# Optimization experiments

Hardware: AMD Instinct MI355X
Metric: run time of the kernel (lower is better)

## Reference

```python
import jax, jax.numpy as jnp
import numpy as np

P = 2        # patch size (all 3 dims)
NB = 8       # num_bands
N = 16       # d_state
DTR = 8      # dt_rank = d_model // 16
DCONV = 4    # d_conv
SMAX = 2.0   # smax_dt = smax_B = smax_C


def _ln(x, g, b):
    mu = x.mean(-1, keepdims=True)
    v = ((x - mu) ** 2).mean(-1, keepdims=True)
    return (x - mu) / jnp.sqrt(v + 1e-5) * g + b


def _silu(x):
    return x * jax.nn.sigmoid(x)


def _ssm_layer(x, band, m, rho, Win, bin_, convw, convb, Wx, Wdt, bdt, Alog, Dp,
               Wout, bout, edt, eB, eC, wr, wm):
    # x: [B, L, d_model] -> bidirectional conditioned selective scan (BiFCSSM)
    Bsz, L, _ = x.shape
    ED = convw.shape[0]
    xz = x @ Win + bin_
    xp, z = xz[..., :ED], xz[..., ED:]
    # depthwise causal conv1d over L
    xpad = jnp.pad(xp, ((0, 0), (DCONV - 1, 0), (0, 0)))
    xc = sum(xpad[:, k:k + L, :] * convw[:, k] for k in range(DCONV)) + convb
    xc = _silu(xc)
    dbl = xc @ Wx                                    # [B,L,DTR+2N]
    dt = jax.nn.softplus(dbl[..., :DTR] @ Wdt + bdt)  # [B,L,ED]
    # band/radius/mask conditioned modulation of delta, B, C
    s_dt = SMAX * jax.nn.sigmoid(edt[band][None] + wr[0] * rho[None] + wm[0] * m)
    s_B = SMAX * jax.nn.sigmoid(eB[band][None] + wr[1] * rho[None] + wm[1] * m)
    s_C = SMAX * jax.nn.sigmoid(eC[band][None] + wr[2] * rho[None] + wm[2] * m)
    dt = dt * s_dt[..., None]
    Bm = dbl[..., DTR:DTR + N] * s_B[..., None]       # [B,L,N]
    Cm = dbl[..., DTR + N:] * s_C[..., None]          # [B,L,N]
    A = -jnp.exp(Alog)                                # [ED,N]
    dA = jnp.exp(dt[..., None] * A)                   # [B,L,ED,N]
    dBu = (dA - 1.0) / A * Bm[:, :, None, :] * xc[..., None]   # exact ZOH
    dA_s = jnp.moveaxis(dA, 1, 0)
    dBu_s = jnp.moveaxis(dBu, 1, 0)
    C_s = jnp.moveaxis(Cm, 1, 0)
    h0 = jnp.zeros((Bsz, ED, N), x.dtype)

    def step(h, inp):
        a, bu, c = inp
        h = a * h + bu
        return h, jnp.einsum('ben,bn->be', h, c)

    _, yf = jax.lax.scan(step, h0, (dA_s, dBu_s, C_s))
    _, yb = jax.lax.scan(step, h0, (dA_s, dBu_s, C_s), reverse=True)
    y = jnp.moveaxis(yf + yb, 0, 1) + Dp * xc
    y = y * _silu(z)
    return y @ Wout + bout


def _fwd(kspace_ri, mask, pe_w, pe_b, pu_w, pu_b, ln_g, ln_b, fn_g, fn_b,
         cond_band, cond_rad_w, cond_mask_w, l0_Win, l0_bin, l0_convw, l0_convb,
         l0_Wx, l0_Wdt, l0_bdt, l0_Alog, l0_D, l0_Wout, l0_bout, l0_edt, l0_eB,
         l0_eC, l0_wr, l0_wm):
    Bsz, C, nx, ny, nz = kspace_ri.shape
    gx, gy, gz = nx // P, ny // P, nz // P
    L = gx * gy * gz
    # patch embed (Conv3d, kernel==stride) as blocked einsum
    xr = kspace_ri.reshape(Bsz, C, gx, P, gy, P, gz, P)
    x = jnp.einsum('bcxiyjzk,dcijk->bdxyz', xr, pe_w) + pe_b[None, :, None, None, None]
    DM = x.shape[1]
    x = x.reshape(Bsz, DM, L).transpose(0, 2, 1)               # [B,L,D]
    m = mask.reshape(Bsz, 1, gx, P, gy, P, gz, P).mean(axis=(3, 5, 7)).reshape(Bsz, L)
    m = jnp.clip(m, 0.0, 1.0)
    # raster scan ordering: identity permutation, rho_bar, band ids
    rho = jnp.arange(L, dtype=x.dtype) / float(L - 1)
    band = jnp.clip(jnp.floor(rho * NB).astype(jnp.int32), 0, NB - 1)
    # condition tokens
    cond = cond_band[band][None] + rho[None, :, None] * cond_rad_w + m[:, :, None] * cond_mask_w
    h = _ln(x + cond, ln_g, ln_b)
    h = h + _ssm_layer(_ln(h, fn_g, fn_b), band, m, rho, l0_Win, l0_bin, l0_convw,
                       l0_convb, l0_Wx, l0_Wdt, l0_bdt, l0_Alog, l0_D, l0_Wout,
                       l0_bout, l0_edt, l0_eB, l0_eC, l0_wr, l0_wm)
    # patch unembed (ConvTranspose3d, kernel==stride) as blocked einsum
    hg = h.transpose(0, 2, 1).reshape(Bsz, DM, gx, gy, gz)
    out = jnp.einsum('bdxyz,dcijk->bcxiyjzk', hg, pu_w).reshape(Bsz, C, nx, ny, nz)
    out = out + pu_b[None, :, None, None, None]
    return kspace_ri + out


def setup_inputs() -> dict:
    key = jax.random.key(0)
    ks = jax.random.split(key, 24)
    ED, DM, CIN = 256, 128, 16

    def nrm(k, shape, s):
        return jax.random.normal(k, shape, jnp.float32) * s

    return {
        'kspace_ri': jax.random.normal(ks[0], (1, CIN, 64, 64, 16), jnp.float32),
        'mask': jax.random.uniform(ks[1], (1, 1, 64, 64, 16), jnp.float32),
        'pe_w': nrm(ks[2], (DM, CIN, P, P, P), 0.09),
        'pe_b': nrm(ks[3], (DM,), 0.02),
        'pu_w': nrm(ks[4], (DM, CIN, P, P, P), 0.05),
        'pu_b': jnp.zeros((CIN,), jnp.float32),
        'ln_g': jnp.ones((DM,), jnp.float32),
        'ln_b': jnp.zeros((DM,), jnp.float32),
        'fn_g': jnp.ones((DM,), jnp.float32),
        'fn_b': jnp.zeros((DM,), jnp.float32),
        'cond_band': nrm(ks[5], (NB, DM), 0.02),
        'cond_rad_w': nrm(ks[6], (DM,), 0.02),
        'cond_mask_w': nrm(ks[7], (DM,), 0.02),
        'l0_Win': nrm(ks[8], (DM, 2 * ED), 0.05),
        'l0_bin': jnp.zeros((2 * ED,), jnp.float32),
        'l0_convw': nrm(ks[9], (ED, DCONV), 0.2),
        'l0_convb': jnp.zeros((ED,), jnp.float32),
        'l0_Wx': nrm(ks[10], (ED, DTR + 2 * N), 0.05),
        'l0_Wdt': nrm(ks[11], (DTR, ED), 0.1),
        'l0_bdt': jnp.full((ED,), -3.0, jnp.float32),
        'l0_Alog': jnp.log(jnp.tile(jnp.arange(1, N + 1, dtype=jnp.float32), (ED, 1))),
        'l0_D': jnp.ones((ED,), jnp.float32),
        'l0_Wout': nrm(ks[12], (ED, DM), 0.05),
        'l0_bout': jnp.zeros((DM,), jnp.float32),
        'l0_edt': nrm(ks[13], (NB,), 0.1),
        'l0_eB': nrm(ks[14], (NB,), 0.1),
        'l0_eC': nrm(ks[15], (NB,), 0.1),
        'l0_wr': nrm(ks[16], (3,), 0.1),
        'l0_wm': nrm(ks[17], (3,), 0.1),
    }


def reference(kspace_ri, mask, pe_w, pe_b, pu_w, pu_b, ln_g, ln_b, fn_g, fn_b,
              cond_band, cond_rad_w, cond_mask_w, l0_Win, l0_bin, l0_convw,
              l0_convb, l0_Wx, l0_Wdt, l0_bdt, l0_Alog, l0_D, l0_Wout, l0_bout,
              l0_edt, l0_eB, l0_eC, l0_wr, l0_wm):
    return _fwd(kspace_ri, mask, pe_w, pe_b, pu_w, pu_b, ln_g, ln_b, fn_g, fn_b,
                cond_band, cond_rad_w, cond_mask_w, l0_Win, l0_bin, l0_convw,
                l0_convb, l0_Wx, l0_Wdt, l0_bdt, l0_Alog, l0_D, l0_Wout, l0_bout,
                l0_edt, l0_eB, l0_eC, l0_wr, l0_wm)
```

## Files before the change

kernel.cpp:

```cpp
#include <hip/hip_runtime.h>
#include <hip/hip_bf16.h>

#define L_TOK 8192
#define NCh 256
#define CLh 32
#define LOG2E 1.44269504088896f

typedef short bf16x8 __attribute__((ext_vector_type(8)));
typedef float f32x4 __attribute__((ext_vector_type(4)));

static __device__ __forceinline__ float nexp2(float x) {
#if __has_builtin(__builtin_amdgcn_exp2f)
    return __builtin_amdgcn_exp2f(x);
#else
    return exp2f(x);
#endif
}
static __device__ __forceinline__ float sigm(float x) {
    return 1.f / (1.f + nexp2(-x * LOG2E));
}
static __device__ __forceinline__ ushort f2bf(float x) {
    union { float f; uint u; } v; v.f = x;
    uint r = v.u + 0x7fffu + ((v.u >> 16) & 1u);
    return (ushort)(r >> 16);
}
static __device__ __forceinline__ float bf2f(ushort h) {
    union { float f; uint u; } v; v.u = ((uint)h) << 16;
    return v.f;
}
static __device__ __forceinline__ void f2hl(float x, ushort* hi, ushort* lo) {
    ushort h = f2bf(x);
    *hi = h;
    *lo = f2bf(x - bf2f(h));
}

#define W_PE   0
#define W_WIN  16384
#define W_WOUT 81920
#define W_PU   114688
#define W_PROJ 131072
#define W_TOT  212992

__global__ __launch_bounds__(256) void prep_k(const float* __restrict__ pe_w, const float* __restrict__ Win,
                                              const float* __restrict__ Wx, const float* __restrict__ Wdt,
                                              const float* __restrict__ Wout, const float* __restrict__ pu_w,
                                              const float* __restrict__ mask,
                                              ushort* __restrict__ wH, ushort* __restrict__ wL,
                                              float* __restrict__ mbuf) {
    int b = blockIdx.x;
    if (b >= 832) {
        int l = (b - 832) * 256 + threadIdx.x;
        int xg = l >> 8, yg = (l >> 3) & 31, zg = l & 7;
        float s = 0.f;
        for (int i2 = 0; i2 < 2; ++i2)
            for (int j2 = 0; j2 < 2; ++j2)
                for (int k2 = 0; k2 < 2; ++k2)
                    s += mask[(2 * xg + i2) * 1024 + (2 * yg + j2) * 16 + 2 * zg + k2];
        s *= 0.125f;
        mbuf[l] = fminf(fmaxf(s, 0.f), 1.f);
        return;
    }
    int i = b * 256 + threadIdx.x;
    float v;
    if (i < 16384) {
        v = pe_w[i];
    } else if (i < 81920) {
        int j = i - 16384; int n = j >> 7, k = j & 127;
        v = Win[k * 512 + n];
    } else if (i < 114688) {
        int j = i - 81920; int n = j >> 8, k = j & 255;
        v = Wout[k * 128 + n];
    } else if (i < 131072) {
        int j = i - 114688; int n = j >> 7, k = j & 127;
        v = pu_w[k * 128 + n];
    } else {
        int j = i - 131072; int n = j >> 8, k = j & 255;
        if (n < 256) {
            float s = 0.f;
#pragma unroll
            for (int r = 0; r < 8; ++r) s += Wx[k * 40 + r] * Wdt[r * 256 + n];
            v = s;
        } else if (n < 288) {
            v = Wx[k * 40 + 8 + (n - 256)];
        } else {
            v = 0.f;
        }
    }
    ushort h, lo; f2hl(v, &h, &lo);
    wH[i] = h; wL[i] = lo;
}

__global__ __launch_bounds__(256) void embed_ln_k(const float* __restrict__ ks,
                                                  const ushort* __restrict__ wH, const ushort* __restrict__ wL,
                                                  const float* __restrict__ pe_b, const float* __restrict__ cond_band,
                                                  const float* __restrict__ cond_rad, const float* __restrict__ cond_mask,
                                                  const float* __restrict__ mbuf,
                                                  const float* __restrict__ ln_g, const float* __restrict__ ln_b,
                                                  const float* __restrict__ fn_g, const float* __restrict__ fn_b,
                                                  float* __restrict__ h_,
                                                  ushort* __restrict__ hnH, ushort* __restrict__ hnL) {
    __shared__ __align__(16) char smem[50176];
    ushort (*AsH)[72] = (ushort(*)[72])(smem);
    ushort (*AsL)[72] = (ushort(*)[72])(smem + 2304);
    ushort (*BsH)[72] = (ushort(*)[72])(smem + 4608);
    ushort (*BsL)[72] = (ushort(*)[72])(smem + 23040);
    float*  ksb       = (float*)(smem + 41472);
    float  (*Cs)[132] = (float(*)[132])(smem);

    const int tid = threadIdx.x;
    const int lane = tid & 63, wn = tid >> 6;
    const int ln = lane & 15, q = lane >> 4;
    const int mb = blockIdx.x * 16;
    const int xg = mb >> 8, yg0 = (mb >> 3) & 31;

    for (int v = tid; v < 512; v += 256) {
        int seg = v >> 2, zq = v & 3;
        int cc = seg >> 3, i2 = (seg >> 2) & 1, yy = seg & 3;
        float4 t4 = *(const float4*)&ks[cc * 65536 + (2 * xg + i2) * 1024 + (2 * yg0 + yy) * 16 + zq * 4];
        int la = seg * 17 + zq * 4;
        ksb[la] = t4.x; ksb[la + 1] = t4.y; ksb[la + 2] = t4.z; ksb[la + 3] = t4.w;
    }

    f32x4 acc[2];
    acc[0] = (f32x4){0.f, 0.f, 0.f, 0.f};
    acc[1] = (f32x4){0.f, 0.f, 0.f, 0.f};

    for (int kc = 0; kc < 128; kc += 64) {
        __syncthreads();
        for (int u = tid; u < 1024; u += 256) {
            int r = u >> 6, kk = u & 63;
            int k = kc + kk;
            int cc = k >> 3, ijk = k & 7;
            int i2 = (ijk >> 2) & 1, j2 = (ijk >> 1) & 1, k2 = ijk & 1;
            int seg = (cc * 2 + i2) * 4 + (r >> 3) * 2 + j2;
            float v = ksb[seg * 17 + (r & 7) * 2 + k2];
            ushort hh, ll; f2hl(v, &hh, &ll);
            AsH[r][kk] = hh; AsL[r][kk] = ll;
        }
        for (int u = tid; u < 1024; u += 256) {
            int n = u >> 3, g = u & 7;
            *(uint4*)&BsH[n][g * 8] = *(const uint4*)&wH[W_PE + n * 128 + kc + g * 8];
            *(uint4*)&BsL[n][g * 8] = *(const uint4*)&wL[W_PE + n * 128 + kc + g * 8];
        }
        __syncthreads();
#pragma unroll
        for (int ks_ = 0; ks_ < 64; ks_ += 32) {
            const int kk = ks_ + q * 8;
            bf16x8 ah = *(const bf16x8*)&AsH[ln][kk];
            bf16x8 al = *(const bf16x8*)&AsL[ln][kk];
#pragma unroll
            for (int cb = 0; cb < 2; ++cb) {
                bf16x8 bh = *(const bf16x8*)&BsH[wn * 32 + cb * 16 + ln][kk];
                bf16x8 bl = *(const bf16x8*)&BsL[wn * 32 + cb * 16 + ln][kk];
                acc[cb] = __builtin_amdgcn_mfma_f32_16x16x32_bf16(ah, bh, acc[cb], 0, 0, 0);
                acc[cb] = __builtin_amdgcn_mfma_f32_16x16x32_bf16(ah, bl, acc[cb], 0, 0, 0);
                acc[cb] = __builtin_amdgcn_mfma_f32_16x16x32_bf16(al, bh, acc[cb], 0, 0, 0);
            }
        }
    }
    __syncthreads();
#pragma unroll
    for (int cb = 0; cb < 2; ++cb) {
#pragma unroll
        for (int r = 0; r < 4; ++r) {
            int row = q * 4 + r;
            int col = wn * 32 + cb * 16 + ln;
            int l = mb + row;
            float rho = (float)l * (1.0f / 8191.0f);
            int band = min(7, (int)(rho * 8.0f));
            Cs[row][col] = acc[cb][r] + pe_b[col] + cond_band[band * 128 + col]
                           + rho * cond_rad[col] + mbuf[l] * cond_mask[col];
        }
    }
    __syncthreads();
    {
        int row = tid >> 4, j = tid & 15;
        int l = mb + row;
        float v8[8];
        float s = 0.f, s2 = 0.f;
#pragma unroll
        for (int i = 0; i < 8; ++i) {
            float v = Cs[row][j * 8 + i];
            v8[i] = v; s += v; s2 += v * v;
        }
#pragma unroll
        for (int o = 1; o < 16; o <<= 1) { s += __shfl_xor(s, o, 16); s2 += __shfl_xor(s2, o, 16); }
        float mu = s * (1.f / 128.f);
        float var = s2 * (1.f / 128.f) - mu * mu;
        float rstd = rsqrtf(fmaxf(var, 0.f) + 1e-5f);
        float hv[8];
        s = 0.f; s2 = 0.f;
#pragma unroll
        for (int i = 0; i < 8; ++i) {
            int col = j * 8 + i;
            float h = (v8[i] - mu) * rstd * ln_g[col] + ln_b[col];
            hv[i] = h; s += h; s2 += h * h;
        }
#pragma unroll
        for (int i = 0; i < 8; i += 4)
            *(float4*)&h_[(size_t)l * 128 + j * 8 + i] = make_float4(hv[i], hv[i + 1], hv[i + 2], hv[i + 3]);
#pragma unroll
        for (int o = 1; o < 16; o <<= 1) { s += __shfl_xor(s, o, 16); s2 += __shfl_xor(s2, o, 16); }
        mu = s * (1.f / 128.f);
        var = s2 * (1.f / 128.f) - mu * mu;
        rstd = rsqrtf(fmaxf(var, 0.f) + 1e-5f);
        union { ushort u[8]; uint4 v4; } oh, ol;
#pragma unroll
        for (int i = 0; i < 8; ++i) {
            int col = j * 8 + i;
            float o2 = (hv[i] - mu) * rstd * fn_g[col] + fn_b[col];
            ushort hh, ll; f2hl(o2, &hh, &ll);
            oh.u[i] = hh; ol.u[i] = ll;
        }
        *(uint4*)&hnH[(size_t)l * 128 + j * 8] = oh.v4;
        *(uint4*)&hnL[(size_t)l * 128 + j * 8] = ol.v4;
    }
}

__global__ __launch_bounds__(256) void win_k(const ushort* __restrict__ Ah, const ushort* __restrict__ Al,
                                             const ushort* __restrict__ wH, const ushort* __restrict__ wL,
                                             const float* __restrict__ bin_,
                                             float* __restrict__ xp, float* __restrict__ sz) {
    __shared__ ushort AsH[64][72], AsL[64][72];
    __shared__ ushort BsH[64][72], BsL[64][72];
    const int tid = threadIdx.x;
    const int lane = tid & 63, wave = tid >> 6;
    const int wm = wave & 1, wn = wave >> 1;
    const int ln = lane & 15, q = lane >> 4;
    const int mb = blockIdx.x * 64, nb = blockIdx.y * 64;

    f32x4 acc[2][2];
#pragma unroll
    for (int rb = 0; rb < 2; ++rb)
#pragma unroll
        for (int cb = 0; cb < 2; ++cb) acc[rb][cb] = (f32x4){0.f, 0.f, 0.f, 0.f};

    for (int kc = 0; kc < 128; kc += 64) {
        __syncthreads();
        for (int u = tid; u < 512; u += 256) {
            int r = u >> 3, g = u & 7;
            size_t go = (size_t)(mb + r) * 128 + kc + g * 8;
            *(uint4*)&AsH[r][g * 8] = *(const uint4*)&Ah[go];
            *(uint4*)&AsL[r][g * 8] = *(const uint4*)&Al[go];
        }
        for (int u = tid; u < 512; u += 256) {
            int n = u >> 3, g = u & 7;
            size_t go = (size_t)(W_WIN) + (size_t)(nb + n) * 128 + kc + g * 8;
            *(uint4*)&BsH[n][g * 8] = *(const uint4*)&wH[go];
            *(uint4*)&BsL[n][g * 8] = *(const uint4*)&wL[go];
        }
        __syncthreads();
#pragma unroll
        for (int ks_ = 0; ks_ < 64; ks_ += 32) {
            const int kk = ks_ + q * 8;
            bf16x8 ah[2], al[2], bh[2], bl[2];
#pragma unroll
            for (int rb = 0; rb < 2; ++rb) {
                ah[rb] = *(const bf16x8*)&AsH[wm * 32 + rb * 16 + ln][kk];
                al[rb] = *(const bf16x8*)&AsL[wm * 32 + rb * 16 + ln][kk];
            }
#pragma unroll
            for (int cb = 0; cb < 2; ++cb) {
                bh[cb] = *(const bf16x8*)&BsH[wn * 32 + cb * 16 + ln][kk];
                bl[cb] = *(const bf16x8*)&BsL[wn * 32 + cb * 16 + ln][kk];
            }
#pragma unroll
            for (int rb = 0; rb < 2; ++rb)
#pragma unroll
                for (int cb = 0; cb < 2; ++cb) {
                    acc[rb][cb] = __builtin_amdgcn_mfma_f32_16x16x32_bf16(ah[rb], bh[cb], acc[rb][cb], 0, 0, 0);
                    acc[rb][cb] = __builtin_amdgcn_mfma_f32_16x16x32_bf16(ah[rb], bl[cb], acc[rb][cb], 0, 0, 0);
                    acc[rb][cb] = __builtin_amdgcn_mfma_f32_16x16x32_bf16(al[rb], bh[cb], acc[rb][cb], 0, 0, 0);
                }
        }
    }
#pragma unroll
    for (int rb = 0; rb < 2; ++rb)
#pragma unroll
        for (int cb = 0; cb < 2; ++cb)
#pragma unroll
            for (int r = 0; r < 4; ++r) {
                int l = mb + wm * 32 + rb * 16 + q * 4 + r;
                int col = nb + wn * 32 + cb * 16 + ln;
                float v = acc[rb][cb][r] + bin_[col];
                if (col < 256) {
                    xp[(size_t)l * 256 + col] = v;
                } else {
                    sz[(size_t)l * 256 + (col - 256)] = v * sigm(v);
                }
            }
}

__global__ __launch_bounds__(512) void proj_k(const float* __restrict__ xp,
                                              const float* __restrict__ convw, const float* __restrict__ convb,
                                              const ushort* __restrict__ wH, const ushort* __restrict__ wL,
                                              const float* __restrict__ bdt, const float* __restrict__ mbuf,
                                              const float* __restrict__ edt, const float* __restrict__ eB,
                                              const float* __restrict__ eC, const float* __restrict__ wr,
                                              const float* __restrict__ wm,
                                              float* __restrict__ xc, float* __restrict__ dt,
                                              float* __restrict__ Bm, float* __restrict__ Cm) {
    __shared__ __align__(16) char smem[52224];
    ushort (*AsH)[264] = (ushort(*)[264])(smem);
    ushort (*AsL)[264] = (ushort(*)[264])(smem + 16896);
    ushort (*BsH)[72]  = (ushort(*)[72])(smem + 33792);
    ushort (*BsL)[72]  = (ushort(*)[72])(smem + 43008);
    const int tid = threadIdx.x;
    const int mb = blockIdx.x * 32;

    {
        const int cg = tid & 63;
        const int rg = tid >> 6;
        const int c0 = cg * 4;
        float4 cb4 = *(const float4*)&convb[c0];
        float4 cw0 = *(const float4*)&convw[(c0 + 0) * 4];
        float4 cw1 = *(const float4*)&convw[(c0 + 1) * 4];
        float4 cw2 = *(const float4*)&convw[(c0 + 2) * 4];
        float4 cw3 = *(const float4*)&convw[(c0 + 3) * 4];
        const int lbase = mb + rg * 4;
        float4 zero = make_float4(0.f, 0.f, 0.f, 0.f);
        float4 x0 = (lbase - 3 >= 0) ? *(const float4*)&xp[(size_t)(lbase - 3) * 256 + c0] : zero;
        float4 x1 = (lbase - 2 >= 0) ? *(const float4*)&xp[(size_t)(lbase - 2) * 256 + c0] : zero;
        float4 x2 = (lbase - 1 >= 0) ? *(const float4*)&xp[(size_t)(lbase - 1) * 256 + c0] : zero;
#pragma unroll
        for (int rr = 0; rr < 4; ++rr) {
            int l = lbase + rr;
            float4 x3 = *(const float4*)&xp[(size_t)l * 256 + c0];
            float o0 = cb4.x + x0.x * cw0.x + x1.x * cw0.y + x2.x * cw0.z + x3.x * cw0.w;
            float o1 = cb4.y + x0.y * cw1.x + x1.y * cw1.y + x2.y * cw1.z + x3.y * cw1.w;
            float o2 = cb4.z + x0.z * cw2.x + x1.z * cw2.y + x2.z * cw2.z + x3.z * cw2.w;
            float o3 = cb4.w + x0.w * cw3.x + x1.w * cw3.y + x2.w * cw3.z + x3.w * cw3.w;
            o0 *= sigm(o0); o1 *= sigm(o1); o2 *= sigm(o2); o3 *= sigm(o3);
            *(float4*)&xc[(size_t)l * 256 + c0] = make_float4(o0, o1, o2, o3);
            union { ushort u[4]; uint2 v2; } hh, ll;
            f2hl(o0, &hh.u[0], &ll.u[0]); f2hl(o1, &hh.u[1], &ll.u[1]);
            f2hl(o2, &hh.u[2], &ll.u[2]); f2hl(o3, &hh.u[3], &ll.u[3]);
            int row = l - mb;
            *(uint2*)&AsH[row][c0] = hh.v2;
            *(uint2*)&AsL[row][c0] = ll.v2;
            x0 = x1; x1 = x2; x2 = x3;
        }
    }
    __syncthreads();

    const int lane = tid & 63, wave = tid >> 6;
    const int wm2 = wave & 1, wn4 = wave >> 1;
    const int ln = lane & 15, q = lane >> 4;
    for (int it = 0; it < 5; ++it) {
        int nb = it * 64;
        f32x4 acc = (f32x4){0.f, 0.f, 0.f, 0.f};
        for (int kc = 0; kc < 256; kc += 64) {
            __syncthreads();
            {
                int u = tid;
                int n = u >> 3, g = u & 7;
                size_t go = (size_t)(W_PROJ) + (size_t)(nb + n) * 256 + kc + g * 8;
                *(uint4*)&BsH[n][g * 8] = *(const uint4*)&wH[go];
                *(uint4*)&BsL[n][g * 8] = *(const uint4*)&wL[go];
            }
            __syncthreads();
#pragma unroll
            for (int ks_ = 0; ks_ < 64; ks_ += 32) {
                const int kka = kc + ks_ + q * 8;
                const int kkb = ks_ + q * 8;
                bf16x8 ah = *(const bf16x8*)&AsH[wm2 * 16 + ln][kka];
                bf16x8 al = *(const bf16x8*)&AsL[wm2 * 16 + ln][kka];
                bf16x8 bh = *(const bf16x8*)&BsH[wn4 * 16 + ln][kkb];
                bf16x8 bl = *(const bf16x8*)&BsL[wn4 * 16 + ln][kkb];
                acc = __builtin_amdgcn_mfma_f32_16x16x32_bf16(ah, bh, acc, 0, 0, 0);
                acc = __builtin_amdgcn_mfma_f32_16x16x32_bf16(ah, bl, acc, 0, 0, 0);
                acc = __builtin_amdgcn_mfma_f32_16x16x32_bf16(al, bh, acc, 0, 0, 0);
            }
        }
#pragma unroll
        for (int r = 0; r < 4; ++r) {
            int l = mb + wm2 * 16 + q * 4 + r;
            int col = nb + wn4 * 16 + ln;
            float v = acc[r];
            float rho = (float)l * (1.0f / 8191.0f);
            int band = min(7, (int)(rho * 8.0f));
            float mv = mbuf[l];
            if (col < 256) {
                float sc0 = 2.0f * sigm(edt[band] + wr[0] * rho + wm[0] * mv);
                float v2 = v + bdt[col];
                float sp = (v2 > 20.f) ? v2 : log1pf(expf(v2));
                dt[(size_t)l * 256 + col] = sp * sc0;
            } else if (col < 272) {
                float sc1 = 2.0f * sigm(eB[band] + wr[1] * rho + wm[1] * mv);
                Bm[(size_t)l * 16 + (col - 256)] = v * sc1;
            } else if (col < 288) {
                float sc2 = 2.0f * sigm(eC[band] + wr[2] * rho + wm[2] * mv);
                Cm[(size_t)l * 16 + (col - 272)] = v * sc2;
            }
        }
    }
}

__global__ __launch_bounds__(256) void scan0_k(const float* __restrict__ dt, const float* __restrict__ xc,
                                               const float* __restrict__ Bm, const float* __restrict__ Alog,
                                               float* __restrict__ Hb, float* __restrict__ sdtb) {
    const int c = blockIdx.x, dir = blockIdx.y, e = threadIdx.x;
    __shared__ float bms[CLh][16];
    for (int idx = e; idx < CLh * 16; idx += 256)
        bms[idx >> 4][idx & 15] = Bm[c * (CLh * 16) + idx];
    float A2[16], iv[16], h[16];
#pragma unroll
    for (int n = 0; n < 16; ++n) {
        float ea = nexp2(Alog[e * 16 + n] * LOG2E);
        A2[n] = -ea * LOG2E;
        iv[n] = -1.0f / ea;
        h[n] = 0.f;
    }
    const int base = c * CLh;
    float cu[8], cx[8], nu[8], nx[8];
#pragma unroll
    for (int j = 0; j < 8; ++j) {
        int p = dir ? (CLh - 1 - j) : j;
        cu[j] = dt[(size_t)(base + p) * 256 + e];
        cx[j] = xc[(size_t)(base + p) * 256 + e];
    }
    __syncthreads();
    float sdt = 0.f;
#pragma unroll
    for (int g = 0; g < CLh / 8; ++g) {
        if (g + 1 < CLh / 8) {
#pragma unroll
            for (int j = 0; j < 8; ++j) {
                int s = (g + 1) * 8 + j;
                int p = dir ? (CLh - 1 - s) : s;
                nu[j] = dt[(size_t)(base + p) * 256 + e];
                nx[j] = xc[(size_t)(base + p) * 256 + e];
            }
        }
#pragma unroll
        for (int j = 0; j < 8; ++j) {
            int s = g * 8 + j;
            int p = dir ? (CLh - 1 - s) : s;
            float u = cu[j], xv = cx[j];
            union { float4 v[4]; float f[16]; } bb;
            const float4* bp = (const float4*)&bms[p][0];
            bb.v[0] = bp[0]; bb.v[1] = bp[1]; bb.v[2] = bp[2]; bb.v[3] = bp[3];
#pragma unroll
            for (int n = 0; n < 16; ++n) {
                float a = nexp2(A2[n] * u);
                float w = xv * bb.f[n] * iv[n];
                h[n] = a * (h[n] + w) - w;
            }
            sdt += u;
        }
#pragma unroll
        for (int j = 0; j < 8; ++j) { cu[j] = nu[j]; cx[j] = nx[j]; }
    }
    const size_t hofs = (size_t)(dir * NCh + c) * 4096 + e * 16;
#pragma unroll
    for (int j = 0; j < 4; ++j)
        *(float4*)&Hb[hofs + 4 * j] = make_float4(h[4 * j], h[4 * j + 1], h[4 * j + 2], h[4 * j + 3]);
    if (dir == 0) sdtb[c * 256 + e] = sdt;
}

__global__ __launch_bounds__(64) void combine_k(const float* __restrict__ Hb, float* __restrict__ Hpre,
                                                const float* __restrict__ sdtb, const float* __restrict__ Alog) {
    int id = blockIdx.x * 64 + threadIdx.x;
    int dir = id >> 12, en = id & 4095, e = en >> 4;
    float A2 = -nexp2(Alog[en] * LOG2E) * LOG2E;
    float hi = 0.f;
    for (int g = 0; g < NCh / 8; ++g) {
        float Pv[8], qv[8];
#pragma unroll
        for (int j = 0; j < 8; ++j) {
            int c = dir ? (NCh - 1 - (g * 8 + j)) : (g * 8 + j);
            Pv[j] = sdtb[c * 256 + e];
            qv[j] = Hb[(size_t)(dir * NCh + c) * 4096 + en];
        }
#pragma unroll
        for (int j = 0; j < 8; ++j) {
            int c = dir ? (NCh - 1 - (g * 8 + j)) : (g * 8 + j);
            float P = nexp2(A2 * Pv[j]);
            Hpre[(size_t)(dir * NCh + c) * 4096 + en] = hi;
            hi = P * hi + qv[j];
        }
    }
}

template <int DIR>
static __device__ __forceinline__ void scan_dir(const float* __restrict__ dt, const float* __restrict__ xc,
                                                int base, int e,
                                                const float (*bms)[16], const float (*cms)[16],
                                                const float* A2, const float* iv,
                                                float* h, float* yreg) {
    float cu[8], cx[8], nu[8], nx[8];
#pragma unroll
    for (int j = 0; j < 8; ++j) {
        const int p = DIR ? (CLh - 1 - j) : j;
        cu[j] = dt[(size_t)(base + p) * 256 + e];
        cx[j] = xc[(size_t)(base + p) * 256 + e];
    }
#pragma unroll
    for (int g = 0; g < CLh / 8; ++g) {
        if (g + 1 < CLh / 8) {
#pragma unroll
            for (int j = 0; j < 8; ++j) {
                const int s = (g + 1) * 8 + j;
                const int p = DIR ? (CLh - 1 - s) : s;
                nu[j] = dt[(size_t)(base + p) * 256 + e];
                nx[j] = xc[(size_t)(base + p) * 256 + e];
            }
        }
#pragma unroll
        for (int j = 0; j < 8; ++j) {
            const int s = g * 8 + j;
            const int p = DIR ? (CLh - 1 - s) : s;
            float u = cu[j], xv = cx[j];
            union { float4 v[4]; float f[16]; } bb, cc;
            const float4* bp = (const float4*)&bms[p][0];
            bb.v[0] = bp[0]; bb.v[1] = bp[1]; bb.v[2] = bp[2]; bb.v[3] = bp[3];
            const float4* cp = (const float4*)&cms[p][0];
            cc.v[0] = cp[0]; cc.v[1] = cp[1]; cc.v[2] = cp[2]; cc.v[3] = cp[3];
            float y = 0.f;
#pragma unroll
            for (int n = 0; n < 16; ++n) {
                float a = nexp2(A2[n] * u);
                float w = xv * bb.f[n] * iv[n];
                h[n] = a * (h[n] + w) - w;
                y += h[n] * cc.f[n];
            }
            yreg[p] = y;
        }
#pragma unroll
        for (int j = 0; j < 8; ++j) { cu[j] = nu[j]; cx[j] = nx[j]; }
    }
}

__global__ __launch_bounds__(512) void scan1g_k(const float* __restrict__ dt, const float* __restrict__ xc,
                                                const float* __restrict__ Bm, const float* __restrict__ Cm,
                                                const float* __restrict__ Alog, const float* __restrict__ Hpre,
                                                const float* __restrict__ sz, const float* __restrict__ Dp,
                                                ushort* __restrict__ AHo, ushort* __restrict__ ALo) {
    const int c = blockIdx.x;
    const int tid = threadIdx.x;
    const int dir = tid >> 8;
    const int e = tid & 255;
    __shared__ float bms[CLh][16];
    __shared__ float cms[CLh][16];
    __shared__ float ysum[CLh][256];
    for (int idx = tid; idx < CLh * 16; idx += 512) {
        bms[idx >> 4][idx & 15] = Bm[c * (CLh * 16) + idx];
        cms[idx >> 4][idx & 15] = Cm[c * (CLh * 16) + idx];
    }
    float A2[16], iv[16], h[16];
#pragma unroll
    for (int n = 0; n < 16; ++n) {
        float ea = nexp2(Alog[e * 16 + n] * LOG2E);
        A2[n] = -ea * LOG2E;
        iv[n] = -1.0f / ea;
    }
    const size_t hofs = (size_t)(dir * NCh + c) * 4096 + e * 16;
#pragma unroll
    for (int j = 0; j < 4; ++j) {
        float4 hv = *(const float4*)&Hpre[hofs + 4 * j];
        h[4 * j] = hv.x; h[4 * j + 1] = hv.y; h[4 * j + 2] = hv.z; h[4 * j + 3] = hv.w;
    }
    const int base = c * CLh;
    float yreg[CLh];
    __syncthreads();
    if (dir == 0) {
        scan_dir<0>(dt, xc, base, e, bms, cms, A2, iv, h, yreg);
    } else {
        scan_dir<1>(dt, xc, base, e, bms, cms, A2, iv, h, yreg);
    }
    __syncthreads();
    if (dir == 0) {
#pragma unroll
        for (int l = 0; l < CLh; ++l) ysum[l][e] = yreg[l];
    }
    __syncthreads();
    if (dir == 1) {
        float dpv = Dp[e];
#pragma unroll
        for (int l = 0; l < CLh; ++l) {
            size_t gl = (size_t)(base + l) * 256 + e;
            float a = (ysum[l][e] + yreg[l] + dpv * xc[gl]) * sz[gl];
            ushort hh, ll; f2hl(a, &hh, &ll);
            AHo[gl] = hh; ALo[gl] = ll;
        }
    }
}

__global__ __launch_bounds__(256) void wout_k(const ushort* __restrict__ AH, const ushort* __restrict__ AL,
                                              const ushort* __restrict__ wH, const ushort* __restrict__ wL,
                                              const float* __restrict__ bout, const float* __restrict__ h_,
                                              ushort* __restrict__ hfH, ushort* __restrict__ hfL) {
    __shared__ ushort AsH[32][72], AsL[32][72];
    __shared__ ushort BsH[64][72], BsL[64][72];
    const int tid = threadIdx.x;
    const int lane = tid & 63, wave = tid >> 6;
    const int wm = wave & 1, wn = wave >> 1;
    const int ln = lane & 15, q = lane >> 4;
    const int mb = blockIdx.x * 32, nb = blockIdx.y * 64;

    f32x4 acc[2];
    acc[0] = (f32x4){0.f, 0.f, 0.f, 0.f};
    acc[1] = (f32x4){0.f, 0.f, 0.f, 0.f};

    for (int kc = 0; kc < 256; kc += 64) {
        __syncthreads();
        for (int u = tid; u < 256; u += 256) {
            int r = u >> 3, g = u & 7;
            size_t go = (size_t)(mb + r) * 256 + kc + g * 8;
            *(uint4*)&AsH[r][g * 8] = *(const uint4*)&AH[go];
            *(uint4*)&AsL[r][g * 8] = *(const uint4*)&AL[go];
        }
        for (int u = tid; u < 512; u += 256) {
            int n = u >> 3, g = u & 7;
            size_t go = (size_t)(W_WOUT) + (size_t)(nb + n) * 256 + kc + g * 8;
            *(uint4*)&BsH[n][g * 8] = *(const uint4*)&wH[go];
            *(uint4*)&BsL[n][g * 8] = *(const uint4*)&wL[go];
        }
        __syncthreads();
#pragma unroll
        for (int ks_ = 0; ks_ < 64; ks_ += 32) {
            const int kk = ks_ + q * 8;
            bf16x8 ah = *(const bf16x8*)&AsH[wm * 16 + ln][kk];
            bf16x8 al = *(const bf16x8*)&AsL[wm * 16 + ln][kk];
#pragma unroll
            for (int cb = 0; cb < 2; ++cb) {
                bf16x8 bh = *(const bf16x8*)&BsH[wn * 32 + cb * 16 + ln][kk];
                bf16x8 bl = *(const bf16x8*)&BsL[wn * 32 + cb * 16 + ln][kk];
                acc[cb] = __builtin_amdgcn_mfma_f32_16x16x32_bf16(ah, bh, acc[cb], 0, 0, 0);
                acc[cb] = __builtin_amdgcn_mfma_f32_16x16x32_bf16(ah, bl, acc[cb], 0, 0, 0);
                acc[cb] = __builtin_amdgcn_mfma_f32_16x16x32_bf16(al, bh, acc[cb], 0, 0, 0);
            }
        }
    }
#pragma unroll
    for (int cb = 0; cb < 2; ++cb)
#pragma unroll
        for (int r = 0; r < 4; ++r) {
            int l = mb + wm * 16 + q * 4 + r;
            int col = nb + wn * 32 + cb * 16 + ln;
            float v = acc[cb][r] + bout[col] + h_[(size_t)l * 128 + col];
            ushort hh, ll; f2hl(v, &hh, &ll);
            hfH[(size_t)l * 128 + col] = hh;
            hfL[(size_t)l * 128 + col] = ll;
        }
}

__global__ __launch_bounds__(256) void unembed_k(const ushort* __restrict__ Ah, const ushort* __restrict__ Al,
                                                 const ushort* __restrict__ wH, const ushort* __restrict__ wL,
                                                 const float* __restrict__ pu_b, const float* __restrict__ ks,
                                                 float* __restrict__ out) {
    __shared__ ushort AsH[32][72], AsL[32][72];
    __shared__ ushort BsH[64][72], BsL[64][72];
    const int tid = threadIdx.x;
    const int lane = tid & 63, wave = tid >> 6;
    const int wm = wave & 1, wn = wave >> 1;
    const int ln = lane & 15, q = lane >> 4;
    const int mb = blockIdx.x * 32, nb = blockIdx.y * 64;

    f32x4 acc[2];
    acc[0] = (f32x4){0.f, 0.f, 0.f, 0.f};
    acc[1] = (f32x4){0.f, 0.f, 0.f, 0.f};

    for (int kc = 0; kc < 128; kc += 64) {
        __syncthreads();
        for (int u = tid; u < 256; u += 256) {
            int r = u >> 3, g = u & 7;
            size_t go = (size_t)(mb + r) * 128 + kc + g * 8;
            *(uint4*)&AsH[r][g * 8] = *(const uint4*)&Ah[go];
            *(uint4*)&AsL[r][g * 8] = *(const uint4*)&Al[go];
        }
        for (int u = tid; u < 512; u += 256) {
            int n = u >> 3, g = u & 7;
            size_t go = (size_t)(W_PU) + (size_t)(nb + n) * 128 + kc + g * 8;
            *(uint4*)&BsH[n][g * 8] = *(const uint4*)&wH[go];
            *(uint4*)&BsL[n][g * 8] = *(const uint4*)&wL[go];
        }
        __syncthreads();
#pragma unroll
        for (int ks_ = 0; ks_ < 64; ks_ += 32) {
            const int kk = ks_ + q * 8;
            bf16x8 ah = *(const bf16x8*)&AsH[wm * 16 + ln][kk];
            bf16x8 al = *(const bf16x8*)&AsL[wm * 16 + ln][kk];
#pragma unroll
            for (int cb = 0; cb < 2; ++cb) {
                bf16x8 bh = *(const bf16x8*)&BsH[wn * 32 + cb * 16 + ln][kk];
                bf16x8 bl = *(const bf16x8*)&BsL[wn * 32 + cb * 16 + ln][kk];
                acc[cb] = __builtin_amdgcn_mfma_f32_16x16x32_bf16(ah, bh, acc[cb], 0, 0, 0);
                acc[cb] = __builtin_amdgcn_mfma_f32_16x16x32_bf16(ah, bl, acc[cb], 0, 0, 0);
                acc[cb] = __builtin_amdgcn_mfma_f32_16x16x32_bf16(al, bh, acc[cb], 0, 0, 0);
            }
        }
    }
#pragma unroll
    for (int cb = 0; cb < 2; ++cb)
#pragma unroll
        for (int r = 0; r < 4; ++r) {
            int l = mb + wm * 16 + q * 4 + r;
            int col = nb + wn * 32 + cb * 16 + ln;
            int xg = l >> 8, yg = (l >> 3) & 31, zg = l & 7;
            int c = col >> 3, ijk = col & 7;
            int i2 = (ijk >> 2) & 1, j2 = (ijk >> 1) & 1, k2 = ijk & 1;
            size_t idx = (size_t)((c * 64 + 2 * xg + i2) * 64 + (2 * yg + j2)) * 16 + 2 * zg + k2;
            out[idx] = acc[cb][r] + pu_b[c] + ks[idx];
        }
}

extern "C" void kernel_launch(void* const* d_in, const int* in_sizes, int n_in,
                              void* d_out, int out_size, void* d_ws, size_t ws_size,
                              hipStream_t stream) {
    const float* ks    = (const float*)d_in[0];
    const float* mask  = (const float*)d_in[1];
    const float* pe_w  = (const float*)d_in[2];
    const float* pe_b  = (const float*)d_in[3];
    const float* pu_w  = (const float*)d_in[4];
    const float* pu_b  = (const float*)d_in[5];
    const float* ln_g  = (const float*)d_in[6];
    const float* ln_b  = (const float*)d_in[7];
    const float* fn_g  = (const float*)d_in[8];
    const float* fn_b  = (const float*)d_in[9];
    const float* cond_band = (const float*)d_in[10];
    const float* cond_rad  = (const float*)d_in[11];
    const float* cond_mask = (const float*)d_in[12];
    const float* Win   = (const float*)d_in[13];
    const float* bin_  = (const float*)d_in[14];
    const float* convw = (const float*)d_in[15];
    const float* convb = (const float*)d_in[16];
    const float* Wx    = (const float*)d_in[17];
    const float* Wdt   = (const float*)d_in[18];
    const float* bdt   = (const float*)d_in[19];
    const float* Alog  = (const float*)d_in[20];
    const float* Dp    = (const float*)d_in[21];
    const float* Wout  = (const float*)d_in[22];
    const float* bout  = (const float*)d_in[23];
    const float* edt   = (const float*)d_in[24];
    const float* eB    = (const float*)d_in[25];
    const float* eC    = (const float*)d_in[26];
    const float* wr    = (const float*)d_in[27];
    const float* wm    = (const float*)d_in[28];
    float* out = (float*)d_out;

    char* base = (char*)d_ws;
    size_t o = 0;
    auto alloc = [&](size_t bytes) { char* p = base + o; o += (bytes + 255) & ~(size_t)255; return p; };
    float*  mbuf = (float*)alloc(32768);
    ushort* wH   = (ushort*)alloc(W_TOT * 2);
    ushort* wL   = (ushort*)alloc(W_TOT * 2);
    float*  h_   = (float*)alloc(4194304);
    ushort* hnH  = (ushort*)alloc(2097152);
    ushort* hnL  = (ushort*)alloc(2097152);
    float*  xp   = (float*)alloc(8388608);
    float*  sz   = (float*)alloc(8388608);
    float*  xc   = (float*)alloc(8388608);
    float*  dt   = (float*)alloc(8388608);
    float*  Bm   = (float*)alloc(524288);
    float*  Cm   = (float*)alloc(524288);
    float*  Hb   = (float*)alloc(8388608);
    float*  Hpre = (float*)alloc(8388608);
    float*  sdtb = (float*)alloc(262144);
    ushort* AHo  = (ushort*)alloc(4194304);
    ushort* ALo  = (ushort*)alloc(4194304);
    ushort* hfH  = (ushort*)alloc(2097152);
    ushort* hfL  = (ushort*)alloc(2097152);

    prep_k<<<864, 256, 0, stream>>>(pe_w, Win, Wx, Wdt, Wout, pu_w, mask, wH, wL, mbuf);
    embed_ln_k<<<512, 256, 0, stream>>>(ks, wH, wL, pe_b, cond_band, cond_rad, cond_mask, mbuf,
                                        ln_g, ln_b, fn_g, fn_b, h_, hnH, hnL);
    win_k<<<dim3(128, 8), 256, 0, stream>>>(hnH, hnL, wH, wL, bin_, xp, sz);
    proj_k<<<256, 512, 0, stream>>>(xp, convw, convb, wH, wL, bdt, mbuf, edt, eB, eC, wr, wm,
                                    xc, dt, Bm, Cm);
    scan0_k<<<dim3(NCh, 2), 256, 0, stream>>>(dt, xc, Bm, Alog, Hb, sdtb);
    combine_k<<<128, 64, 0, stream>>>(Hb, Hpre, sdtb, Alog);
    scan1g_k<<<NCh, 512, 0, stream>>>(dt, xc, Bm, Cm, Alog, Hpre, sz, Dp, AHo, ALo);
    wout_k<<<dim3(256, 2), 256, 0, stream>>>(AHo, ALo, wH, wL, bout, h_, hfH, hfL);
    unembed_k<<<dim3(256, 2), 256, 0, stream>>>(hfH, hfL, wH, wL, pu_b, ks, out);
}
```

Before: 236.6 us.

## Fuse Wout projection and unembed GEMMs into one kernel via LDS staging

Merges the output projection (y@Wout + bias + residual) and the patch unembed GEMM into a single kernel with 512 threads per block covering all 128 output columns. The full 32x256 A tile is loaded once into LDS, and the hidden result is kept in LDS as a hi/lo bf16 split instead of going through global buffers. This removes one kernel launch, the global round trip of the intermediate, and the duplicated A loads across the former y-dimension blocks. The cost is about 70KB of LDS per block and fewer blocks (256 instead of 512), which reduces occupancy.

```diff
diff --git a/kernel.cpp b/kernel.cpp
--- a/kernel.cpp
+++ b/kernel.cpp
@@ -586,17 +586,31 @@
     }
 }
 
-__global__ __launch_bounds__(256) void wout_k(const ushort* __restrict__ AH, const ushort* __restrict__ AL,
-                                              const ushort* __restrict__ wH, const ushort* __restrict__ wL,
-                                              const float* __restrict__ bout, const float* __restrict__ h_,
-                                              ushort* __restrict__ hfH, ushort* __restrict__ hfL) {
-    __shared__ ushort AsH[32][72], AsL[32][72];
-    __shared__ ushort BsH[64][72], BsL[64][72];
+__global__ __launch_bounds__(512) void wu_k(const ushort* __restrict__ AH, const ushort* __restrict__ AL,
+                                            const ushort* __restrict__ wH, const ushort* __restrict__ wL,
+                                            const float* __restrict__ bout, const float* __restrict__ h_,
+                                            const float* __restrict__ pu_b, const float* __restrict__ ks,
+                                            float* __restrict__ out) {
+    __shared__ __align__(16) char smem[70656];
+    ushort (*AsH)[264] = (ushort(*)[264])(smem);
+    ushort (*AsL)[264] = (ushort(*)[264])(smem + 16896);
+    ushort (*BsH)[72]  = (ushort(*)[72])(smem + 33792);
+    ushort (*BsL)[72]  = (ushort(*)[72])(smem + 52224);
+    ushort (*hfH)[136] = (ushort(*)[136])(smem);
+    ushort (*hfL)[136] = (ushort(*)[136])(smem + 8704);
+
     const int tid = threadIdx.x;
     const int lane = tid & 63, wave = tid >> 6;
     const int wm = wave & 1, wn = wave >> 1;
     const int ln = lane & 15, q = lane >> 4;
-    const int mb = blockIdx.x * 32, nb = blockIdx.y * 64;
+    const int mb = blockIdx.x * 32;
+
+    for (int u = tid; u < 1024; u += 512) {
+        int r = u >> 5, g = u & 31;
+        size_t go = (size_t)(mb + r) * 256 + g * 8;
+        *(uint4*)&AsH[r][g * 8] = *(const uint4*)&AH[go];
+        *(uint4*)&AsL[r][g * 8] = *(const uint4*)&AL[go];
+    }
 
     f32x4 acc[2];
     acc[0] = (f32x4){0.f, 0.f, 0.f, 0.f};
@@ -604,104 +618,82 @@
 
     for (int kc = 0; kc < 256; kc += 64) {
         __syncthreads();
-        for (int u = tid; u < 256; u += 256) {
-            int r = u >> 3, g = u & 7;
-            size_t go = (size_t)(mb + r) * 256 + kc + g * 8;
-            *(uint4*)&AsH[r][g * 8] = *(const uint4*)&AH[go];
-            *(uint4*)&AsL[r][g * 8] = *(const uint4*)&AL[go];
-        }
-        for (int u = tid; u < 512; u += 256) {
+        for (int u = tid; u < 1024; u += 512) {
             int n = u >> 3, g = u & 7;
-            size_t go = (size_t)(W_WOUT) + (size_t)(nb + n) * 256 + kc + g * 8;
+            size_t go = (size_t)(W_WOUT) + (size_t)n * 256 + kc + g * 8;
             *(uint4*)&BsH[n][g * 8] = *(const uint4*)&wH[go];
             *(uint4*)&BsL[n][g * 8] = *(const uint4*)&wL[go];
         }
         __syncthreads();
 #pragma unroll
         for (int ks_ = 0; ks_ < 64; ks_ += 32) {
-            const int kk = ks_ + q * 8;
-            bf16x8 ah = *(const bf16x8*)&AsH[wm * 16 + ln][kk];
-            bf16x8 al = *(const bf16x8*)&AsL[wm * 16 + ln][kk];
+            const int kka = kc + ks_ + q * 8;
+            const int kkb = ks_ + q * 8;
+            bf16x8 ah = *(const bf16x8*)&AsH[wm * 16 + ln][kka];
+            bf16x8 al = *(const bf16x8*)&AsL[wm * 16 + ln][kka];
 #pragma unroll
             for (int cb = 0; cb < 2; ++cb) {
-                bf16x8 bh = *(const bf16x8*)&BsH[wn * 32 + cb * 16 + ln][kk];
-                bf16x8 bl = *(const bf16x8*)&BsL[wn * 32 + cb * 16 + ln][kk];
+                bf16x8 bh = *(const bf16x8*)&BsH[wn * 32 + cb * 16 + ln][kkb];
+                bf16x8 bl = *(const bf16x8*)&BsL[wn * 32 + cb * 16 + ln][kkb];
                 acc[cb] = __builtin_amdgcn_mfma_f32_16x16x32_bf16(ah, bh, acc[cb], 0, 0, 0);
                 acc[cb] = __builtin_amdgcn_mfma_f32_16x16x32_bf16(ah, bl, acc[cb], 0, 0, 0);
                 acc[cb] = __builtin_amdgcn_mfma_f32_16x16x32_bf16(al, bh, acc[cb], 0, 0, 0);
             }
         }
     }
+    __syncthreads();
+#pragma unroll
+    for (int cb = 0; cb < 2; ++cb)
+#pragma unroll
+        for (int r = 0; r < 4; ++r) {
+            int row = wm * 16 + q * 4 + r;
+            int col = wn * 32 + cb * 16 + ln;
+            float v = acc[cb][r] + bout[col] + h_[(size_t)(mb + row) * 128 + col];
+            ushort hh, ll; f2hl(v, &hh, &ll);
+            hfH[row][col] = hh;
+            hfL[row][col] = ll;
+        }
+    __syncthreads();
+
+    f32x4 acc2[2];
+    acc2[0] = (f32x4){0.f, 0.f, 0.f, 0.f};
+    acc2[1] = (f32x4){0.f, 0.f, 0.f, 0.f};
+    for (int kc = 0; kc < 128; kc += 64) {
+        __syncthreads();
+        for (int u = tid; u < 1024; u += 512) {
+            int n = u >> 3, g = u & 7;
+            size_t go = (size_t)(W_PU) + (size_t)n * 128 + kc + g * 8;
+            *(uint4*)&BsH[n][g * 8] = *(const uint4*)&wH[go];
+            *(uint4*)&BsL[n][g * 8] = *(const uint4*)&wL[go];
+        }
+        __syncthreads();
+#pragma unroll
+        for (int ks_ = 0; ks_ < 64; ks_ += 32) {
+            const int kka = kc + ks_ + q * 8;
+            const int kkb = ks_ + q * 8;
+            bf16x8 ah = *(const bf16x8*)&hfH[wm * 16 + ln][kka];
+            bf16x8 al = *(const bf16x8*)&hfL[wm * 16 + ln][kka];
+#pragma unroll
+            for (int cb = 0; cb < 2; ++cb) {
+                bf16x8 bh = *(const bf16x8*)&BsH[wn * 32 + cb * 16 + ln][kkb];
+                bf16x8 bl = *(const bf16x8*)&BsL[wn * 32 + cb * 16 + ln][kkb];
+                acc2[cb] = __builtin_amdgcn_mfma_f32_16x16x32_bf16(ah, bh, acc2[cb], 0, 0, 0);
+                acc2[cb] = __builtin_amdgcn_mfma_f32_16x16x32_bf16(ah, bl, acc2[cb], 0, 0, 0);
+                acc2[cb] = __builtin_amdgcn_mfma_f32_16x16x32_bf16(al, bh, acc2[cb], 0, 0, 0);
+            }
+        }
+    }
 #pragma unroll
     for (int cb = 0; cb < 2; ++cb)
 #pragma unroll
         for (int r = 0; r < 4; ++r) {
             int l = mb + wm * 16 + q * 4 + r;
-            int col = nb + wn * 32 + cb * 16 + ln;
-            float v = acc[cb][r] + bout[col] + h_[(size_t)l * 128 + col];
-            ushort hh, ll; f2hl(v, &hh, &ll);
-            hfH[(size_t)l * 128 + col] = hh;
-            hfL[(size_t)l * 128 + col] = ll;
-        }
-}
-
-__global__ __launch_bounds__(256) void unembed_k(const ushort* __restrict__ Ah, const ushort* __restrict__ Al,
-                                                 const ushort* __restrict__ wH, const ushort* __restrict__ wL,
-                                                 const float* __restrict__ pu_b, const float* __restrict__ ks,
-                                                 float* __restrict__ out) {
-    __shared__ ushort AsH[32][72], AsL[32][72];
-    __shared__ ushort BsH[64][72], BsL[64][72];
-    const int tid = threadIdx.x;
-    const int lane = tid & 63, wave = tid >> 6;
-    const int wm = wave & 1, wn = wave >> 1;
-    const int ln = lane & 15, q = lane >> 4;
-    const int mb = blockIdx.x * 32, nb = blockIdx.y * 64;
-
-    f32x4 acc[2];
-    acc[0] = (f32x4){0.f, 0.f, 0.f, 0.f};
-    acc[1] = (f32x4){0.f, 0.f, 0.f, 0.f};
-
-    for (int kc = 0; kc < 128; kc += 64) {
-        __syncthreads();
-        for (int u = tid; u < 256; u += 256) {
-            int r = u >> 3, g = u & 7;
-            size_t go = (size_t)(mb + r) * 128 + kc + g * 8;
-            *(uint4*)&AsH[r][g * 8] = *(const uint4*)&Ah[go];
-            *(uint4*)&AsL[r][g * 8] = *(const uint4*)&Al[go];
-        }
-        for (int u = tid; u < 512; u += 256) {
-            int n = u >> 3, g = u & 7;
-            size_t go = (size_t)(W_PU) + (size_t)(nb + n) * 128 + kc + g * 8;
-            *(uint4*)&BsH[n][g * 8] = *(const uint4*)&wH[go];
-            *(uint4*)&BsL[n][g * 8] = *(const uint4*)&wL[go];
-        }
-        __syncthreads();
-#pragma unroll
-        for (int ks_ = 0; ks_ < 64; ks_ += 32) {
-            const int kk = ks_ + q * 8;
-            bf16x8 ah = *(const bf16x8*)&AsH[wm * 16 + ln][kk];
-            bf16x8 al = *(const bf16x8*)&AsL[wm * 16 + ln][kk];
-#pragma unroll
-            for (int cb = 0; cb < 2; ++cb) {
-                bf16x8 bh = *(const bf16x8*)&BsH[wn * 32 + cb * 16 + ln][kk];
-                bf16x8 bl = *(const bf16x8*)&BsL[wn * 32 + cb * 16 + ln][kk];
-                acc[cb] = __builtin_amdgcn_mfma_f32_16x16x32_bf16(ah, bh, acc[cb], 0, 0, 0);
-                acc[cb] = __builtin_amdgcn_mfma_f32_16x16x32_bf16(ah, bl, acc[cb], 0, 0, 0);
-                acc[cb] = __builtin_amdgcn_mfma_f32_16x16x32_bf16(al, bh, acc[cb], 0, 0, 0);
-            }
-        }
-    }
-#pragma unroll
-    for (int cb = 0; cb < 2; ++cb)
-#pragma unroll
-        for (int r = 0; r < 4; ++r) {
-            int l = mb + wm * 16 + q * 4 + r;
-            int col = nb + wn * 32 + cb * 16 + ln;
+            int col = wn * 32 + cb * 16 + ln;
             int xg = l >> 8, yg = (l >> 3) & 31, zg = l & 7;
-            int c = col >> 3, ijk = col & 7;
+            int cch = col >> 3, ijk = col & 7;
             int i2 = (ijk >> 2) & 1, j2 = (ijk >> 1) & 1, k2 = ijk & 1;
-            size_t idx = (size_t)((c * 64 + 2 * xg + i2) * 64 + (2 * yg + j2)) * 16 + 2 * zg + k2;
-            out[idx] = acc[cb][r] + pu_b[c] + ks[idx];
+            size_t idx = (size_t)((cch * 64 + 2 * xg + i2) * 64 + (2 * yg + j2)) * 16 + 2 * zg + k2;
+            out[idx] = acc2[cb][r] + pu_b[cch] + ks[idx];
         }
 }
 
@@ -759,8 +751,6 @@
     float*  sdtb = (float*)alloc(262144);
     ushort* AHo  = (ushort*)alloc(4194304);
     ushort* ALo  = (ushort*)alloc(4194304);
-    ushort* hfH  = (ushort*)alloc(2097152);
-    ushort* hfL  = (ushort*)alloc(2097152);
 
     prep_k<<<864, 256, 0, stream>>>(pe_w, Win, Wx, Wdt, Wout, pu_w, mask, wH, wL, mbuf);
     embed_ln_k<<<512, 256, 0, stream>>>(ks, wH, wL, pe_b, cond_band, cond_rad, cond_mask, mbuf,
@@ -771,6 +761,5 @@
     scan0_k<<<dim3(NCh, 2), 256, 0, stream>>>(dt, xc, Bm, Alog, Hb, sdtb);
     combine_k<<<128, 64, 0, stream>>>(Hb, Hpre, sdtb, Alog);
     scan1g_k<<<NCh, 512, 0, stream>>>(dt, xc, Bm, Cm, Alog, Hpre, sz, Dp, AHo, ALo);
-    wout_k<<<dim3(256, 2), 256, 0, stream>>>(AHo, ALo, wH, wL, bout, h_, hfH, hfL);
-    unembed_k<<<dim3(256, 2), 256, 0, stream>>>(hfH, hfL, wH, wL, pu_b, ks, out);
-}
+    wu_k<<<256, 512, 0, stream>>>(AHo, ALo, wH, wL, bout, h_, pu_b, ks, out);
+}
```

Result: slower. 328.0 us (+38.6%).
